# Kernel optimization log

Measured on AMD Instinct MI355X. Metric: run time of the kernel, lower is better.

The kernel has to match this reference:

```python
import jax, jax.numpy as jnp
import numpy as np

N_NODES = 100000
N_EDGES = 1600000
IN_DIM = 8
EMB = 50
NUM_TASK = 112
NUM_LAYER = 2
BN_EPS = 1e-5


def setup_inputs() -> dict:
    key = jax.random.key(0)
    ks = jax.random.split(key, 12)
    s = 0.1  # weight init scale
    L, D = NUM_LAYER, EMB
    return {
        "src": jax.random.randint(ks[0], (N_EDGES,), 0, N_NODES),
        "dst": jax.random.randint(ks[1], (N_EDGES,), 0, N_NODES),
        "node_feats": jax.random.normal(ks[2], (N_NODES, IN_DIM), jnp.float32),
        "edge_feats": jax.random.normal(ks[3], (N_EDGES, IN_DIM), jnp.float32),
        "node_W": jax.random.normal(ks[4], (IN_DIM, D), jnp.float32) * s,
        "node_b": jnp.zeros((D,), jnp.float32),
        "edge_W": jax.random.normal(ks[5], (IN_DIM, D), jnp.float32) * s,
        "edge_b": jnp.zeros((D,), jnp.float32),
        "eps": jnp.zeros((L,), jnp.float32),
        "W1": jax.random.normal(ks[6], (L, D, 2 * D), jnp.float32) * s,
        "b1": jnp.zeros((L, 2 * D), jnp.float32),
        "g1": jnp.ones((L, 2 * D), jnp.float32),
        "be1": jnp.zeros((L, 2 * D), jnp.float32),
        "W2": jax.random.normal(ks[7], (L, 2 * D, D), jnp.float32) * s,
        "b2": jnp.zeros((L, D), jnp.float32),
        "g2": jnp.ones((L, D), jnp.float32),
        "be2": jnp.zeros((L, D), jnp.float32),
        "pred_W": jax.random.normal(ks[8], (D, NUM_TASK), jnp.float32) * s,
        "pred_b": jnp.zeros((NUM_TASK,), jnp.float32),
    }


def _bn(x, gamma, beta):
    # BatchNorm1d in training mode: batch mean, biased variance, eps=1e-5
    mu = jnp.mean(x, axis=0)
    var = jnp.mean(jnp.square(x - mu), axis=0)
    return (x - mu) * jax.lax.rsqrt(var + BN_EPS) * gamma + beta


def reference(src, dst, node_feats, edge_feats, node_W, node_b, edge_W, edge_b,
              eps, W1, b1, g1, be1, W2, b2, g2, be2, pred_W, pred_b):
    N = node_feats.shape[0]
    h = node_feats @ node_W + node_b          # [N, D] node encoder
    e = edge_feats @ edge_W + edge_b          # [E, D] edge encoder
    deg = jax.ops.segment_sum(jnp.ones(src.shape, h.dtype), dst, num_segments=N)
    inv_deg = jnp.where(deg > 0, 1.0 / jnp.maximum(deg, 1.0), 0.0)[:, None]  # mean; 0 for isolated nodes
    for i in range(W1.shape[0]):
        m = h[src] + e                                          # u_add_e
        agg = jax.ops.segment_sum(m, dst, num_segments=N) * inv_deg  # mean reduce
        h = (1.0 + eps[i]) * h + agg                            # eps-combine
        h = jax.nn.relu(_bn(h @ W1[i] + b1[i], g1[i], be1[i]))
        h = jax.nn.relu(_bn(h @ W2[i] + b2[i], g2[i], be2[i]))
    return h @ pred_W + pred_b                # [N, num_task]
```

## Files before the change

kernel.cpp:

```cpp
#include <hip/hip_runtime.h>
#include <hip/hip_bf16.h>

#define N_NODES 100000
#define N_EDGES 1600000
#define IN_DIM 8
#define D 50
#define D2 100
#define NTASK 112
#define BN_EPS 1e-5f
#define NBLK ((N_NODES + 255) / 256)
#define HS 56
#define SLOT 48

#define PARTS 8
#define NPP (N_NODES / PARTS)
#define SF_BPP 128
typedef int i4 __attribute__((ext_vector_type(4)));
typedef __attribute__((ext_vector_type(8))) short s16x8;
typedef __attribute__((ext_vector_type(4))) float f32x4;

__device__ __forceinline__ unsigned bf16_rn(float x) {
    unsigned u = __float_as_uint(x);
    return (u + 0x7fffu + ((u >> 16) & 1u)) >> 16;
}
__device__ __forceinline__ unsigned pack_bf16(float a, float b) {
    return bf16_rn(a) | (bf16_rn(b) << 16);
}

__global__ __launch_bounds__(256) void node_enc_pair(
    const float* __restrict__ nf, const float* __restrict__ nW,
    const float* __restrict__ nb, float* __restrict__ h,
    unsigned* __restrict__ hb) {
    __shared__ float sW[IN_DIM * D];
    __shared__ float sb[D];
    __shared__ float snf[10 * IN_DIM];
    int t = threadIdx.x;
    int n0 = blockIdx.x * 10;
    for (int i = t; i < IN_DIM * D; i += 256) sW[i] = nW[i];
    for (int i = t; i < D; i += 256) sb[i] = nb[i];
    for (int i = t; i < 10 * IN_DIM; i += 256) {
        int g = n0 * IN_DIM + i;
        snf[i] = (g < N_NODES * IN_DIM) ? nf[g] : 0.0f;
    }
    __syncthreads();
    if (t >= 250) return;
    int n = t / 25, j2 = t % 25;
    int g = n0 + n;
    if (g >= N_NODES) return;
    int j0 = 2 * j2, j1 = j0 + 1;
    float v0 = sb[j0], v1 = sb[j1];
#pragma unroll
    for (int k = 0; k < IN_DIM; k++) {
        float f = snf[n * IN_DIM + k];
        v0 += f * sW[k * D + j0];
        v1 += f * sW[k * D + j1];
    }
    *(float2*)&h[(size_t)g * HS + j0] = make_float2(v0, v1);
    if (hb) hb[(size_t)g * 32 + j2] = pack_bf16(v0, v1);
}

__global__ __launch_bounds__(256) void k_slotfill_part(
    const int* __restrict__ src, const int* __restrict__ dst,
    int* __restrict__ degi, int2* __restrict__ slots) {
    const int part = blockIdx.x & (PARTS - 1);
    const int blk = blockIdx.x >> 3;
    const int lo = part * NPP, hi = lo + NPP;
    const int NT = SF_BPP * 256;
    const int NG = N_EDGES / 4;
    const i4* s4 = (const i4*)src;
    const i4* d4 = (const i4*)dst;
    for (int g = blk * 256 + (int)threadIdx.x; g < NG; g += NT) {
        i4 dd = __builtin_nontemporal_load(d4 + g);
        i4 ss = __builtin_nontemporal_load(s4 + g);
#pragma unroll
        for (int k = 0; k < 4; k++) {
            int d = dd[k];
            if (d >= lo && d < hi) {
                int pos = atomicAdd(&degi[d], 1);
                if (pos < SLOT) slots[(size_t)d * SLOT + pos] = make_int2(ss[k], 4 * g + k);
            }
        }
    }
}

__global__ __launch_bounds__(256) void k_aggef_slot(
    const int* __restrict__ degi, const int2* __restrict__ slots,
    const float* __restrict__ ef, float* __restrict__ aggef) {
    int lane = threadIdx.x & 63, wv = threadIdx.x >> 6;
    int n = (blockIdx.x & 7) * NPP + (blockIdx.x >> 3) * 4 + wv;
    if (n >= N_NODES) return;
    int deg = degi[n];
    if (deg > SLOT) deg = SLOT;
    int g = lane >> 3, k = lane & 7;
    float a = 0.0f;
    for (int q = g; q < deg; q += 8) {
        int e = slots[(size_t)n * SLOT + q].y;
        a += ef[(size_t)e * 8 + k];
    }
    a += __shfl_xor(a, 8, 64);
    a += __shfl_xor(a, 16, 64);
    a += __shfl_xor(a, 32, 64);
    if (lane < 8) aggef[(size_t)n * 8 + lane] = a;
}

template<bool USE_HB>
__global__ __launch_bounds__(256) void gather_slot(
    const int* __restrict__ degi, const int2* __restrict__ slots,
    const float* __restrict__ aggef, const float* __restrict__ eW,
    const float* __restrict__ eb, const float* __restrict__ h,
    const unsigned* __restrict__ hb, const float* __restrict__ epsArr,
    int layer, float* __restrict__ hnew) {
    __shared__ float sW[IN_DIM * D];
    __shared__ float sB[D];
    int t = threadIdx.x;
    for (int i = t; i < IN_DIM * D; i += 256) sW[i] = eW[i];
    for (int i = t; i < D; i += 256) sB[i] = eb[i];
    __syncthreads();
    int lane = t & 63, wv = t >> 6, half = lane >> 5, li = lane & 31;
    int part = blockIdx.x & 7, bi = blockIdx.x >> 3;
    int r = bi * 8 + wv * 2 + half;
    if (r >= NPP) return;
    int n = part * NPP + r;
    int deg = degi[n];
    if (deg > SLOT) deg = SLOT;
    float iv = (deg > 0) ? (1.0f / (float)deg) : 0.0f;
    const int2* srow = &slots[(size_t)n * SLOT];
    float ax0 = 0, ay0 = 0, ax1 = 0, ay1 = 0;
    int p = 0;
    if (USE_HB) {
        for (; p + 8 <= deg; p += 8) {
            int4 q0 = *(const int4*)&srow[p];
            int4 q1 = *(const int4*)&srow[p + 2];
            int4 q2 = *(const int4*)&srow[p + 4];
            int4 q3 = *(const int4*)&srow[p + 6];
            if (li < 25) {
                unsigned w;
                w = hb[(size_t)q0.x * 32 + li]; ax0 += __uint_as_float(w << 16); ay0 += __uint_as_float(w & 0xffff0000u);
                w = hb[(size_t)q0.z * 32 + li]; ax1 += __uint_as_float(w << 16); ay1 += __uint_as_float(w & 0xffff0000u);
                w = hb[(size_t)q1.x * 32 + li]; ax0 += __uint_as_float(w << 16); ay0 += __uint_as_float(w & 0xffff0000u);
                w = hb[(size_t)q1.z * 32 + li]; ax1 += __uint_as_float(w << 16); ay1 += __uint_as_float(w & 0xffff0000u);
                w = hb[(size_t)q2.x * 32 + li]; ax0 += __uint_as_float(w << 16); ay0 += __uint_as_float(w & 0xffff0000u);
                w = hb[(size_t)q2.z * 32 + li]; ax1 += __uint_as_float(w << 16); ay1 += __uint_as_float(w & 0xffff0000u);
                w = hb[(size_t)q3.x * 32 + li]; ax0 += __uint_as_float(w << 16); ay0 += __uint_as_float(w & 0xffff0000u);
                w = hb[(size_t)q3.z * 32 + li]; ax1 += __uint_as_float(w << 16); ay1 += __uint_as_float(w & 0xffff0000u);
            }
        }
        if (p < deg) {
            int4 q0 = *(const int4*)&srow[p];
            int4 q1 = *(const int4*)&srow[p + 2];
            int4 q2 = *(const int4*)&srow[p + 4];
            int4 q3 = *(const int4*)&srow[p + 6];
            if (li < 25) {
                unsigned w;
                w = hb[(size_t)q0.x * 32 + li]; ax0 += __uint_as_float(w << 16); ay0 += __uint_as_float(w & 0xffff0000u);
                if (p + 1 < deg) { w = hb[(size_t)q0.z * 32 + li]; ax1 += __uint_as_float(w << 16); ay1 += __uint_as_float(w & 0xffff0000u); }
                if (p + 2 < deg) { w = hb[(size_t)q1.x * 32 + li]; ax0 += __uint_as_float(w << 16); ay0 += __uint_as_float(w & 0xffff0000u); }
                if (p + 3 < deg) { w = hb[(size_t)q1.z * 32 + li]; ax1 += __uint_as_float(w << 16); ay1 += __uint_as_float(w & 0xffff0000u); }
                if (p + 4 < deg) { w = hb[(size_t)q2.x * 32 + li]; ax0 += __uint_as_float(w << 16); ay0 += __uint_as_float(w & 0xffff0000u); }
                if (p + 5 < deg) { w = hb[(size_t)q2.z * 32 + li]; ax1 += __uint_as_float(w << 16); ay1 += __uint_as_float(w & 0xffff0000u); }
                if (p + 6 < deg) { w = hb[(size_t)q3.x * 32 + li]; ax0 += __uint_as_float(w << 16); ay0 += __uint_as_float(w & 0xffff0000u); }
            }
        }
    } else {
        for (; p < deg; p += 4) {
            int4 q0 = *(const int4*)&srow[p];
            int4 q1 = *(const int4*)&srow[p + 2];
            if (li < 25) {
                float2 v = *(const float2*)&h[(size_t)q0.x * HS + 2 * li];
                ax0 += v.x; ay0 += v.y;
                if (p + 1 < deg) {
                    v = *(const float2*)&h[(size_t)q0.z * HS + 2 * li];
                    ax1 += v.x; ay1 += v.y;
                }
                if (p + 2 < deg) {
                    v = *(const float2*)&h[(size_t)q1.x * HS + 2 * li];
                    ax0 += v.x; ay0 += v.y;
                }
                if (p + 3 < deg) {
                    v = *(const float2*)&h[(size_t)q1.z * HS + 2 * li];
                    ax1 += v.x; ay1 += v.y;
                }
            }
        }
    }
    if (li < 25) {
        float accx = ax0 + ax1, accy = ay0 + ay1;
        int j0 = 2 * li, j1 = j0 + 1;
        float e0 = 0.0f, e1 = 0.0f;
        if (deg > 0) {
            const float* ag = &aggef[(size_t)n * 8];
            float s0 = 0.0f, s1 = 0.0f;
#pragma unroll
            for (int k = 0; k < 8; k++) {
                float a = ag[k];
                s0 += a * sW[k * D + j0];
                s1 += a * sW[k * D + j1];
            }
            e0 = s0 * iv + sB[j0];
            e1 = s1 * iv + sB[j1];
        }
        float epsv = 1.0f + epsArr[layer];
        float2 hv = *(const float2*)&h[(size_t)n * HS + j0];
        float2 o;
        o.x = epsv * hv.x + iv * accx + e0;
        o.y = epsv * hv.y + iv * accy + e1;
        *(float2*)&hnew[(size_t)n * D + j0] = o;
    }
}

template<int K, int KP, int J, int JP, bool BN_IN, bool STATS>
__global__ __launch_bounds__(256) void gemm_mfma(
    const float* __restrict__ X, const float* __restrict__ W,
    const float* __restrict__ bias,
    const float* __restrict__ bnS, const float* __restrict__ bnQ,
    const float* __restrict__ bnG, const float* __restrict__ bnB,
    float* __restrict__ Y, float* __restrict__ sg, float* __restrict__ qg,
    int ntiles) {
    constexpr int RB = 64;
    constexpr int WS = KP + 8;
    constexpr int KS = KP / 32;
    constexpr int NCT = JP / 16;
    constexpr bool RAGGED = (N_NODES % RB) != 0;
    __shared__ __align__(16) unsigned short shA_hi[RB * WS];
    __shared__ __align__(16) unsigned short shA_lo[RB * WS];
    __shared__ __align__(16) unsigned short sWT_hi[JP * WS];
    __shared__ __align__(16) unsigned short sWT_lo[JP * WS];
    __shared__ float sb[JP];
    __shared__ float sa[BN_IN ? K : 1], sc[BN_IN ? K : 1];
    __shared__ float sp[JP], qp[JP];
    int t = threadIdx.x;
    for (int i = t; i < RB * WS; i += 256) { shA_hi[i] = 0; shA_lo[i] = 0; }
    for (int i = t; i < JP * WS; i += 256) { sWT_hi[i] = 0; sWT_lo[i] = 0; }
    __syncthreads();
    for (int i = t; i < KP * JP; i += 256) {
        int k = i / JP, j = i % JP;
        float v = (k < K && j < J) ? W[k * J + j] : 0.0f;
        unsigned hv = bf16_rn(v);
        float hf = __uint_as_float(hv << 16);
        sWT_hi[j * WS + k] = (unsigned short)hv;
        sWT_lo[j * WS + k] = (unsigned short)bf16_rn(v - hf);
    }
    for (int i = t; i < JP; i += 256) sb[i] = (i < J) ? bias[i] : 0.0f;
    if (BN_IN) {
        const float invN = 1.0f / (float)N_NODES;
        for (int i = t; i < K; i += 256) {
            float mu = bnS[i] * invN;
            float var = bnQ[i] * invN - mu * mu;
            float rs = rsqrtf(var + BN_EPS);
            float a = bnG[i] * rs;
            sa[i] = a;
            sc[i] = bnB[i] - mu * a;
        }
    }
    if (STATS) {
        for (int i = t; i < JP; i += 256) { sp[i] = 0.0f; qp[i] = 0.0f; }
    }
    int lane = t & 63, wv = t >> 6;
    int lrow = lane & 15, lkg = lane >> 4;
    float sacc[NCT], qacc[NCT];
#pragma unroll
    for (int c = 0; c < NCT; c++) { sacc[c] = 0.0f; qacc[c] = 0.0f; }
    for (int tile = blockIdx.x; tile < ntiles; tile += gridDim.x) {
        __syncthreads();
        int base = tile * RB;
        for (int i = t; i < RB * K; i += 256) {
            int r = i / K, k = i % K;
            float v = 0.0f;
            if (!RAGGED || base + r < N_NODES) {
                v = X[(size_t)base * K + i];
                if (BN_IN) v = fmaxf(v * sa[k] + sc[k], 0.0f);
            }
            unsigned hv = bf16_rn(v);
            float hf = __uint_as_float(hv << 16);
            shA_hi[r * WS + k] = (unsigned short)hv;
            shA_lo[r * WS + k] = (unsigned short)bf16_rn(v - hf);
        }
        __syncthreads();
        s16x8 ah[KS], al[KS];
        int arow = wv * 16 + lrow;
#pragma unroll
        for (int ks = 0; ks < KS; ks++) {
            int off = arow * WS + ks * 32 + lkg * 8;
            ah[ks] = *(const s16x8*)&shA_hi[off];
            al[ks] = *(const s16x8*)&shA_lo[off];
        }
#pragma unroll
        for (int ct = 0; ct < NCT; ct++) {
            f32x4 a0 = {0.f, 0.f, 0.f, 0.f};
            f32x4 a1 = {0.f, 0.f, 0.f, 0.f};
            f32x4 a2 = {0.f, 0.f, 0.f, 0.f};
#pragma unroll
            for (int ks = 0; ks < KS; ks++) {
                int boff = (ct * 16 + lrow) * WS + ks * 32 + lkg * 8;
                s16x8 bh = *(const s16x8*)&sWT_hi[boff];
                s16x8 bl = *(const s16x8*)&sWT_lo[boff];
                a0 = __builtin_amdgcn_mfma_f32_16x16x32_bf16(ah[ks], bh, a0, 0, 0, 0);
                a1 = __builtin_amdgcn_mfma_f32_16x16x32_bf16(ah[ks], bl, a1, 0, 0, 0);
                a2 = __builtin_amdgcn_mfma_f32_16x16x32_bf16(al[ks], bh, a2, 0, 0, 0);
            }
            int col = ct * 16 + lrow;
#pragma unroll
            for (int j = 0; j < 4; j++) {
                int gn = base + wv * 16 + lkg * 4 + j;
                if (!RAGGED || gn < N_NODES) {
                    float v = a0[j] + (a1[j] + a2[j]) + sb[col];
                    if (col < J) Y[(size_t)gn * J + col] = v;
                    if (STATS) { sacc[ct] += v; qacc[ct] += v * v; }
                }
            }
        }
    }
    if (STATS) {
        __syncthreads();
#pragma unroll
        for (int c = 0; c < NCT; c++) {
            atomicAdd(&sp[c * 16 + (t & 15)], sacc[c]);
            atomicAdd(&qp[c * 16 + (t & 15)], qacc[c]);
        }
        __syncthreads();
        for (int i = t; i < J; i += 256) {
            atomicAdd(&sg[i], sp[i]);
            atomicAdd(&qg[i], qp[i]);
        }
    }
}

__global__ __launch_bounds__(256) void apply2_pair(
    const float* __restrict__ y2, const float* __restrict__ sr,
    const float* __restrict__ qr, const float* __restrict__ g,
    const float* __restrict__ be, float* __restrict__ h,
    unsigned* __restrict__ hb) {
    __shared__ float sa[D], sc[D];
    int t = threadIdx.x;
    if (t < D) {
        float invN = 1.0f / (float)N_NODES;
        float mu = sr[t] * invN;
        float var = qr[t] * invN - mu * mu;
        float rs = rsqrtf(var + BN_EPS);
        float a = g[t] * rs;
        sa[t] = a;
        sc[t] = be[t] - mu * a;
    }
    __syncthreads();
    int idx = blockIdx.x * 256 + t;
    if (idx >= N_NODES * 25) return;
    int n = idx / 25, j2 = idx % 25;
    int j0 = 2 * j2, j1 = j0 + 1;
    float2 y = *(const float2*)&y2[(size_t)n * D + j0];
    float v0 = fmaxf(y.x * sa[j0] + sc[j0], 0.0f);
    float v1 = fmaxf(y.y * sa[j1] + sc[j1], 0.0f);
    *(float2*)&h[(size_t)n * HS + j0] = make_float2(v0, v1);
    if (hb) hb[(size_t)n * 32 + j2] = pack_bf16(v0, v1);
}

__global__ void k_deg(const int* __restrict__ dst, int* __restrict__ degi) {
    int e = blockIdx.x * blockDim.x + threadIdx.x;
    if (e < N_EDGES) atomicAdd(&degi[dst[e]], 1);
}
__global__ void k_bsum(const int* __restrict__ degi, int* __restrict__ bsum) {
    __shared__ int lds[256];
    int t = threadIdx.x, i = blockIdx.x * 256 + t;
    lds[t] = (i < N_NODES) ? degi[i] : 0;
    __syncthreads();
    for (int s = 128; s > 0; s >>= 1) {
        if (t < s) lds[t] += lds[t + s];
        __syncthreads();
    }
    if (t == 0) bsum[blockIdx.x] = lds[0];
}
__global__ void k_bscan(const int* __restrict__ bsum, int* __restrict__ bpre) {
    __shared__ int lds[512];
    int t = threadIdx.x;
    int x = (t < NBLK) ? bsum[t] : 0;
    lds[t] = x;
    __syncthreads();
    int acc = x;
    for (int s = 1; s < 512; s <<= 1) {
        int add = (t >= s) ? lds[t - s] : 0;
        __syncthreads();
        acc += add;
        lds[t] = acc;
        __syncthreads();
    }
    if (t < NBLK) bpre[t] = acc - x;
}
__global__ void k_off(int* __restrict__ degi, const int* __restrict__ bpre,
                      int* __restrict__ off, float* __restrict__ invd) {
    __shared__ int lds[256];
    int t = threadIdx.x, i = blockIdx.x * 256 + t;
    int dv = (i < N_NODES) ? degi[i] : 0;
    lds[t] = dv;
    __syncthreads();
    int acc = dv;
    for (int s = 1; s < 256; s <<= 1) {
        int add = (t >= s) ? lds[t - s] : 0;
        __syncthreads();
        acc += add;
        lds[t] = acc;
        __syncthreads();
    }
    int excl = acc - dv + bpre[blockIdx.x];
    if (i < N_NODES) {
        off[i] = excl;
        degi[i] = excl;
        invd[i] = (dv > 0) ? (1.0f / (float)dv) : 0.0f;
    }
    if (i == 0) off[N_NODES] = N_EDGES;
}
__global__ void k_fill(const int* __restrict__ src, const int* __restrict__ dst,
                       int* __restrict__ cursor, int2* __restrict__ adj) {
    int e = blockIdx.x * blockDim.x + threadIdx.x;
    if (e >= N_EDGES) return;
    int d = dst[e];
    int pos = atomicAdd(&cursor[d], 1);
    adj[pos] = make_int2(src[e], e);
}
__global__ __launch_bounds__(256) void k_aggef_csr(
    const int* __restrict__ off, const int2* __restrict__ adj,
    const float* __restrict__ ef, float* __restrict__ aggef) {
    int lane = threadIdx.x & 63, wv = threadIdx.x >> 6;
    int n = blockIdx.x * 4 + wv;
    if (n >= N_NODES) return;
    int p0 = off[n], pend = off[n + 1];
    int g = lane >> 3, k = lane & 7;
    float a = 0.0f;
    for (int q = p0 + g; q < pend; q += 8) a += ef[(size_t)adj[q].y * 8 + k];
    a += __shfl_xor(a, 8, 64);
    a += __shfl_xor(a, 16, 64);
    a += __shfl_xor(a, 32, 64);
    if (lane < 8) aggef[(size_t)n * 8 + lane] = a;
}
__global__ __launch_bounds__(256) void gather_csr(
    const int* __restrict__ off, const int2* __restrict__ adj,
    const float* __restrict__ aggef, const float* __restrict__ eW,
    const float* __restrict__ eb, const float* __restrict__ h,
    const float* __restrict__ invd, const float* __restrict__ epsArr,
    int layer, float* __restrict__ hnew) {
    __shared__ float sW[IN_DIM * D];
    __shared__ float sB[D];
    int t = threadIdx.x;
    for (int i = t; i < IN_DIM * D; i += 256) sW[i] = eW[i];
    for (int i = t; i < D; i += 256) sB[i] = eb[i];
    __syncthreads();
    int lane = t & 63, wv = t >> 6;
    int n = blockIdx.x * 4 + wv;
    if (n >= N_NODES) return;
    int dd = (lane < D) ? lane : (D - 1);
    int p = off[n], pend = off[n + 1];
    int deg = pend - p;
    float acc = 0.0f;
    while (p + 4 <= pend) {
        int s0 = adj[p].x, s1 = adj[p + 1].x, s2 = adj[p + 2].x, s3 = adj[p + 3].x;
        acc += h[(size_t)s0 * HS + dd] + h[(size_t)s1 * HS + dd]
             + h[(size_t)s2 * HS + dd] + h[(size_t)s3 * HS + dd];
        p += 4;
    }
    while (p < pend) { acc += h[(size_t)adj[p].x * HS + dd]; p++; }
    if (lane < D) {
        float iv = invd[n];
        float extra = 0.0f;
        if (deg > 0) {
            const float* ag = &aggef[(size_t)n * 8];
            float s = 0.0f;
#pragma unroll
            for (int k = 0; k < 8; k++) s += ag[k] * sW[k * D + dd];
            extra = s * iv + sB[dd];
        }
        float epsv = 1.0f + epsArr[layer];
        hnew[(size_t)n * D + lane] = epsv * h[(size_t)n * HS + lane] + iv * acc + extra;
    }
}

extern "C" void kernel_launch(void* const* d_in, const int* in_sizes, int n_in,
                              void* d_out, int out_size, void* d_ws, size_t ws_size,
                              hipStream_t stream) {
    const int*   src        = (const int*)d_in[0];
    const int*   dst        = (const int*)d_in[1];
    const float* node_feats = (const float*)d_in[2];
    const float* edge_feats = (const float*)d_in[3];
    const float* node_W     = (const float*)d_in[4];
    const float* node_b     = (const float*)d_in[5];
    const float* edge_W     = (const float*)d_in[6];
    const float* edge_b     = (const float*)d_in[7];
    const float* epsArr     = (const float*)d_in[8];
    const float* W1         = (const float*)d_in[9];
    const float* b1         = (const float*)d_in[10];
    const float* g1         = (const float*)d_in[11];
    const float* be1        = (const float*)d_in[12];
    const float* W2         = (const float*)d_in[13];
    const float* b2         = (const float*)d_in[14];
    const float* g2         = (const float*)d_in[15];
    const float* be2        = (const float*)d_in[16];
    const float* pred_W     = (const float*)d_in[17];
    const float* pred_b     = (const float*)d_in[18];
    float* out = (float*)d_out;

    float* ws = (float*)d_ws;
    unsigned* hb = nullptr;
    float *h, *tmp, *invd = nullptr, *st, *aggef;
    int *degi, *off = nullptr, *bsum = nullptr, *bpre = nullptr;
    int2 *slots = nullptr, *adj = nullptr;

    auto layout = [&](int mode) -> size_t {
        float* p = ws;
        hb = nullptr; slots = nullptr; adj = nullptr;
        off = nullptr; bsum = nullptr; bpre = nullptr; invd = nullptr;
        if (mode == 2) { hb = (unsigned*)p; p += (size_t)N_NODES * 32; }
        h = p;    p += (size_t)N_NODES * HS;
        tmp = p;  p += (size_t)N_NODES * D;
        st = p;   p += 768;
        if (mode == 0) { invd = p; p += N_NODES; }
        int* ip = (int*)p;
        degi = ip; ip += N_NODES;
        char* end;
        if (mode >= 1) {
            slots = (int2*)ip;
            aggef = (float*)(slots + (size_t)N_NODES * SLOT);
            end = (char*)(aggef + (size_t)N_NODES * 8);
        } else {
            off = ip;  ip += N_NODES + 1;
            bsum = ip; ip += NBLK;
            bpre = ip; ip += NBLK + 1;
            adj = (int2*)ip;
            aggef = (float*)(adj + N_EDGES);
            end = (char*)(aggef + (size_t)N_NODES * 8);
        }
        return (size_t)(end - (char*)d_ws);
    };
    int mode = 2;
    if (ws_size < layout(2)) { mode = 1; if (ws_size < layout(1)) { mode = 0; layout(0); } }

    float* s1 = st, *q1 = st + 128, *s2 = st + 256, *q2 = st + 320;
    float* y1 = out;

    node_enc_pair<<<10000, 256, 0, stream>>>(node_feats, node_W, node_b, h, hb);
    hipMemsetAsync(degi, 0, N_NODES * sizeof(int), stream);

    const int GATHER_GRID = PARTS * ((NPP + 7) / 8);
    if (mode >= 1) {
        k_slotfill_part<<<PARTS * SF_BPP, 256, 0, stream>>>(src, dst, degi, slots);
        k_aggef_slot<<<(N_NODES + 3) / 4, 256, 0, stream>>>(degi, slots, edge_feats, aggef);
    } else {
        k_deg<<<(N_EDGES + 255) / 256, 256, 0, stream>>>(dst, degi);
        k_bsum<<<NBLK, 256, 0, stream>>>(degi, bsum);
        k_bscan<<<1, 512, 0, stream>>>(bsum, bpre);
        k_off<<<NBLK, 256, 0, stream>>>(degi, bpre, off, invd);
        k_fill<<<(N_EDGES + 255) / 256, 256, 0, stream>>>(src, dst, degi, adj);
        k_aggef_csr<<<(N_NODES + 3) / 4, 256, 0, stream>>>(off, adj, edge_feats, aggef);
    }

    const int NT64 = (N_NODES + 63) / 64;
    for (int layer = 0; layer < 2; layer++) {
        hipMemsetAsync(st, 0, 384 * sizeof(float), stream);
        if (mode == 2)
            gather_slot<true><<<GATHER_GRID, 256, 0, stream>>>(
                degi, slots, aggef, edge_W, edge_b, h, hb, epsArr, layer, tmp);
        else if (mode == 1)
            gather_slot<false><<<GATHER_GRID, 256, 0, stream>>>(
                degi, slots, aggef, edge_W, edge_b, h, nullptr, epsArr, layer, tmp);
        else
            gather_csr<<<(N_NODES + 3) / 4, 256, 0, stream>>>(
                off, adj, aggef, edge_W, edge_b, h, invd, epsArr, layer, tmp);
        gemm_mfma<50, 64, 100, 112, false, true><<<768, 256, 0, stream>>>(
            tmp, W1 + layer * D * D2, b1 + layer * D2, st, st, st, st, y1, s1, q1, NT64);
        gemm_mfma<100, 128, 50, 64, true, true><<<512, 256, 0, stream>>>(
            y1, W2 + layer * D2 * D, b2 + layer * D,
            s1, q1, g1 + layer * D2, be1 + layer * D2, tmp, s2, q2, NT64);
        if (layer == 0)
            apply2_pair<<<(N_NODES * 25 + 255) / 256, 256, 0, stream>>>(
                tmp, s2, q2, g2, be2, h, hb);
    }
    gemm_mfma<50, 64, 112, 112, true, false><<<768, 256, 0, stream>>>(
        tmp, pred_W, pred_b, s2, q2, g2 + D, be2 + D, out, st, st, NT64);
}
```

Measured before the change: 659.6 us.

## Split slot-fill partitions into subranges and batch atomics; truncate bf16 hi split

The slot-fill kernel now makes two passes per partition, each covering half the node range, so the atomic counters and slot writes touch a smaller working set. Each thread loads two edge groups at once and issues all eight atomics before any slot store, to overlap atomic latency. Non-temporal loads are replaced with plain loads, so the extra pass can reuse edge data from cache but reads src/dst twice. Separately, the bf16 hi/lo split in the GEMM now truncates the high half instead of rounding it, which removes a few ALU ops while the lo term absorbs the residual.

```diff
diff --git a/kernel.cpp b/kernel.cpp
--- a/kernel.cpp
+++ b/kernel.cpp
@@ -15,6 +15,7 @@
 #define PARTS 8
 #define NPP (N_NODES / PARTS)
 #define SF_BPP 128
+#define SUBP 2
 typedef int i4 __attribute__((ext_vector_type(4)));
 typedef __attribute__((ext_vector_type(8))) short s16x8;
 typedef __attribute__((ext_vector_type(4))) float f32x4;
@@ -64,20 +65,46 @@
     int* __restrict__ degi, int2* __restrict__ slots) {
     const int part = blockIdx.x & (PARTS - 1);
     const int blk = blockIdx.x >> 3;
-    const int lo = part * NPP, hi = lo + NPP;
     const int NT = SF_BPP * 256;
     const int NG = N_EDGES / 4;
     const i4* s4 = (const i4*)src;
     const i4* d4 = (const i4*)dst;
-    for (int g = blk * 256 + (int)threadIdx.x; g < NG; g += NT) {
-        i4 dd = __builtin_nontemporal_load(d4 + g);
-        i4 ss = __builtin_nontemporal_load(s4 + g);
-#pragma unroll
-        for (int k = 0; k < 4; k++) {
-            int d = dd[k];
-            if (d >= lo && d < hi) {
-                int pos = atomicAdd(&degi[d], 1);
-                if (pos < SLOT) slots[(size_t)d * SLOT + pos] = make_int2(ss[k], 4 * g + k);
+    const int HALF = NPP / SUBP;
+    for (int sp = 0; sp < SUBP; sp++) {
+        const int lo = part * NPP + sp * HALF, hi = lo + HALF;
+        int g = blk * 256 + (int)threadIdx.x;
+        for (; g + NT < NG; g += 2 * NT) {
+            i4 dd0 = d4[g],      ss0 = s4[g];
+            i4 dd1 = d4[g + NT], ss1 = s4[g + NT];
+            int dv[8], sv[8], ev[8], pos[8];
+#pragma unroll
+            for (int k = 0; k < 4; k++) {
+                dv[k] = dd0[k]; sv[k] = ss0[k]; ev[k] = 4 * g + k;
+                dv[k + 4] = dd1[k]; sv[k + 4] = ss1[k]; ev[k + 4] = 4 * (g + NT) + k;
+            }
+#pragma unroll
+            for (int k = 0; k < 8; k++) {
+                bool a = (dv[k] >= lo && dv[k] < hi);
+                pos[k] = a ? atomicAdd(&degi[dv[k]], 1) : SLOT;
+            }
+#pragma unroll
+            for (int k = 0; k < 8; k++) {
+                if (pos[k] < SLOT)
+                    slots[(size_t)dv[k] * SLOT + pos[k]] = make_int2(sv[k], ev[k]);
+            }
+        }
+        if (g < NG) {
+            i4 dd0 = d4[g], ss0 = s4[g];
+            int pos[4];
+#pragma unroll
+            for (int k = 0; k < 4; k++) {
+                bool a = (dd0[k] >= lo && dd0[k] < hi);
+                pos[k] = a ? atomicAdd(&degi[dd0[k]], 1) : SLOT;
+            }
+#pragma unroll
+            for (int k = 0; k < 4; k++) {
+                if (pos[k] < SLOT)
+                    slots[(size_t)dd0[k] * SLOT + pos[k]] = make_int2(ss0[k], 4 * g + k);
             }
         }
     }
@@ -235,9 +262,9 @@
     for (int i = t; i < KP * JP; i += 256) {
         int k = i / JP, j = i % JP;
         float v = (k < K && j < J) ? W[k * J + j] : 0.0f;
-        unsigned hv = bf16_rn(v);
-        float hf = __uint_as_float(hv << 16);
-        sWT_hi[j * WS + k] = (unsigned short)hv;
+        unsigned u = __float_as_uint(v);
+        float hf = __uint_as_float(u & 0xffff0000u);
+        sWT_hi[j * WS + k] = (unsigned short)(u >> 16);
         sWT_lo[j * WS + k] = (unsigned short)bf16_rn(v - hf);
     }
     for (int i = t; i < JP; i += 256) sb[i] = (i < J) ? bias[i] : 0.0f;
@@ -270,9 +297,9 @@
                 v = X[(size_t)base * K + i];
                 if (BN_IN) v = fmaxf(v * sa[k] + sc[k], 0.0f);
             }
-            unsigned hv = bf16_rn(v);
-            float hf = __uint_as_float(hv << 16);
-            shA_hi[r * WS + k] = (unsigned short)hv;
+            unsigned u = __float_as_uint(v);
+            float hf = __uint_as_float(u & 0xffff0000u);
+            shA_hi[r * WS + k] = (unsigned short)(u >> 16);
             shA_lo[r * WS + k] = (unsigned short)bf16_rn(v - hf);
         }
         __syncthreads();
```

After: 674.1 us. +2.2%, slower.
